# Performance work log

Hardware: AMD Instinct MI355X
Metric: run time of the kernel (lower is better)

The kernel has to match this reference:

```python
import jax, jax.numpy as jnp
import numpy as np

N_NODES = 50000
N_EDGES = 1600000
H_DIM = 128
OUT_DIM = 128
N_RELS = 16


def setup_inputs() -> dict:
    key = jax.random.key(0)
    k1, k2, k3, k4, k5, k6 = jax.random.split(key, 6)
    node_ids = jnp.arange(N_NODES, dtype=jnp.int64) if jax.config.jax_enable_x64 else jnp.arange(N_NODES, dtype=jnp.int32)
    src = jax.random.randint(k1, (N_EDGES,), 0, N_NODES, dtype=jnp.int32)
    dst = jax.random.randint(k2, (N_EDGES,), 0, N_NODES, dtype=jnp.int32)
    rel = jax.random.randint(k3, (N_EDGES,), 0, N_RELS, dtype=jnp.int32)
    norm = jax.random.uniform(k4, (N_EDGES, 1), dtype=jnp.float32)
    emb_table = jax.random.normal(k5, (N_NODES, H_DIM), dtype=jnp.float32)
    W = jax.random.normal(k6, (N_RELS, H_DIM, OUT_DIM), dtype=jnp.float32) * (1.0 / np.sqrt(H_DIM))
    return {"node_ids": node_ids, "src": src, "dst": dst, "rel": rel,
            "norm": norm, "emb_table": emb_table, "W": W}


def reference(node_ids, src, dst, rel, norm, emb_table, W):
    # Input layer: embedding lookup on node ids.  [N, h_dim]
    h = emb_table[node_ids]
    n_nodes = emb_table.shape[0]
    # RelGraphConv (full per-relation weight, no basis, no self-loop,
    # activation=None for the single/last layer, dropout inactive at eval):
    # Transform all node features by every relation weight up front
    # (R small, avoids [E, d, o] per-edge weight gather).  [R, N, out]
    h_rel = jnp.einsum('nd,rdo->rno', h, W)
    # Gather per-edge transformed source features, apply edge norm.  [E, out]
    msg = h_rel[rel, src] * norm
    # Scatter-sum messages to destination nodes.  [N, out]
    out = jax.ops.segment_sum(msg, dst, num_segments=n_nodes)
    return out
```

## Files before the change

kernel.cpp:

```cpp
#include <hip/hip_runtime.h>
#include <hip/hip_bf16.h>

#define NN 50000
#define NE 1600000
#define HD 128
#define NR 16
#define NCB 1563
#define SLOT 2048
#define LASTCAP 1024
#define NMAX 1999
#define PREPH_BLKS 6250
#define PREPW_BLKS 128
#define S2B 512
#define EPB (NE / S2B)

typedef __bf16 bf16x8 __attribute__((ext_vector_type(8)));
typedef unsigned short u16x8 __attribute__((ext_vector_type(8)));
typedef float f32x4 __attribute__((ext_vector_type(4)));

__device__ __forceinline__ unsigned short f2bf(float f) {
    union { float f; unsigned int u; } v; v.f = f;
    unsigned int u = v.u;
    u += 0x7FFFu + ((u >> 16) & 1u);
    return (unsigned short)(u >> 16);
}
__device__ __forceinline__ float bflo(unsigned int u) {
    union { unsigned int u; float f; } v; v.u = u << 16; return v.f;
}
__device__ __forceinline__ float bfhi(unsigned int u) {
    union { unsigned int u; float f; } v; v.u = u & 0xFFFF0000u; return v.f;
}

__global__ __launch_bounds__(256) void prep_all(const int* __restrict__ node_ids,
                                                const float* __restrict__ emb,
                                                unsigned short* __restrict__ h_bf,
                                                const float* __restrict__ W,
                                                unsigned short* __restrict__ Wt,
                                                int* __restrict__ gcur) {
    const int b = blockIdx.x;
    const int t = threadIdx.x;
    if (b < PREPH_BLKS) {
        int gid = b * 256 + t;
        int row = gid >> 5;
        int c = (gid & 31) << 2;
        int nid = node_ids[row];
        if (nid < 0) nid = 0; if (nid >= NN) nid = NN - 1;
        float4 v = *(const float4*)(emb + (size_t)nid * HD + c);
        ushort4 o;
        o.x = f2bf(v.x); o.y = f2bf(v.y); o.z = f2bf(v.z); o.w = f2bf(v.w);
        *(ushort4*)(h_bf + (size_t)row * HD + c) = o;
    } else if (b < PREPH_BLKS + PREPW_BLKS) {
        int gid = (b - PREPH_BLKS) * 256 + t;
        int out8 = gid * 8;
        int r = out8 >> 14;
        int rem = out8 & 16383;
        int o = rem >> 7;
        int k0 = rem & 127;
        const float* wsrc = W + (size_t)r * 16384;
        unsigned short v8[8];
        #pragma unroll
        for (int i = 0; i < 8; ++i)
            v8[i] = f2bf(wsrc[(k0 + i) * 128 + o]);
        *(uint4*)(Wt + (size_t)r * 16384 + (size_t)o * 128 + k0) =
            *(const uint4*)v8;
    } else {
        for (int i = t; i < NCB; i += 256) gcur[i] = 0;
    }
}

__global__ __launch_bounds__(256) void scat2(const int* __restrict__ src,
                                             const int* __restrict__ dst,
                                             const int* __restrict__ rel,
                                             const float* __restrict__ norm,
                                             int* __restrict__ gcur,
                                             uint2* __restrict__ recs) {
    __shared__ int cur[NCB];
    const int t = threadIdx.x, sb = blockIdx.x;
    const int base = sb * EPB;
    for (int i = t; i < NCB; i += 256) cur[i] = 0;
    __syncthreads();
    for (int i = t; i < EPB; i += 256)
        atomicAdd(&cur[((unsigned)dst[base + i]) >> 5], 1);
    __syncthreads();
    for (int i = t; i < NCB; i += 256) {
        int c = cur[i];
        if (c > 0) cur[i] = atomicAdd(&gcur[i], c);
    }
    __syncthreads();
    for (int i = t; i < EPB; i += 256) {
        int e = base + i;
        int d = dst[e];
        int bin = ((unsigned)d) >> 5;
        int p = atomicAdd(&cur[bin], 1);
        int cap = (bin == NCB - 1) ? LASTCAP : SLOT;
        if (p < cap) {
            unsigned x = (unsigned)src[e] | ((unsigned)rel[e] << 16)
                       | ((unsigned)(d & 31) << 20);
            recs[(size_t)bin * SLOT + p] = make_uint2(x, __float_as_uint(norm[e]));
        }
    }
}

__global__ __launch_bounds__(256) void gemm_hrel(const unsigned short* __restrict__ h_bf,
                                                 const unsigned short* __restrict__ Wt,
                                                 unsigned short* __restrict__ h_rel) {
    __shared__ unsigned short sA[128][136];
    __shared__ unsigned short sB[128][136];
    const int t = threadIdx.x;
    const int base = blockIdx.x * 128;
    const int rg = blockIdx.y;

    #pragma unroll
    for (int j = 0; j < 8; ++j) {
        int idx = t + j * 256;
        int row = idx >> 4;
        int c8 = (idx & 15) << 3;
        int g = base + row;
        if (g >= NN) g = 0;
        uint4 v = *(const uint4*)(h_bf + (size_t)g * 128 + c8);
        *(uint4*)&sA[row][c8] = v;
    }

    const int lane = t & 63;
    const int w = t >> 6;
    const int wr = w >> 1, wc = w & 1;
    const int l15 = lane & 15, lhi = lane >> 4;

    for (int rr = 0; rr < 4; ++rr) {
        const int r = rg * 4 + rr;
        if (rr > 0) __syncthreads();
        const unsigned short* wp = Wt + ((size_t)r << 14);
        #pragma unroll
        for (int j = 0; j < 8; ++j) {
            int idx = t + j * 256;
            int row = idx >> 4;
            int c8 = (idx & 15) << 3;
            uint4 v = *(const uint4*)(wp + (size_t)row * 128 + c8);
            *(uint4*)&sB[row][c8] = v;
        }
        __syncthreads();

        f32x4 acc[4][4];
        #pragma unroll
        for (int i = 0; i < 4; ++i)
            #pragma unroll
            for (int j = 0; j < 4; ++j)
                acc[i][j] = (f32x4){0.f, 0.f, 0.f, 0.f};

        #pragma unroll
        for (int kt = 0; kt < 4; ++kt) {
            const int ko = kt * 32 + lhi * 8;
            bf16x8 aF[4], bF[4];
            #pragma unroll
            for (int ms = 0; ms < 4; ++ms) {
                u16x8 raw = *(const u16x8*)&sA[wr * 64 + ms * 16 + l15][ko];
                aF[ms] = __builtin_bit_cast(bf16x8, raw);
            }
            #pragma unroll
            for (int nt = 0; nt < 4; ++nt) {
                u16x8 raw = *(const u16x8*)&sB[wc * 64 + nt * 16 + l15][ko];
                bF[nt] = __builtin_bit_cast(bf16x8, raw);
            }
            #pragma unroll
            for (int ms = 0; ms < 4; ++ms)
                #pragma unroll
                for (int nt = 0; nt < 4; ++nt)
                    acc[ms][nt] = __builtin_amdgcn_mfma_f32_16x16x32_bf16(
                        aF[ms], bF[nt], acc[ms][nt], 0, 0, 0);
        }

        __syncthreads();
        #pragma unroll
        for (int ms = 0; ms < 4; ++ms)
            #pragma unroll
            for (int nt = 0; nt < 4; ++nt)
                #pragma unroll
                for (int reg = 0; reg < 4; ++reg)
                    sB[wr * 64 + ms * 16 + lhi * 4 + reg]
                      [wc * 64 + nt * 16 + l15] = f2bf(acc[ms][nt][reg]);
        __syncthreads();
        size_t rbase = ((size_t)r * NN + base) * 128;
        #pragma unroll
        for (int j = 0; j < 8; ++j) {
            int idx = t + j * 256;
            int row = idx >> 4;
            int c8 = (idx & 15) << 3;
            if (base + row < NN) {
                uint4 v = *(const uint4*)&sB[row][c8];
                *(uint4*)(h_rel + rbase + (size_t)row * 128 + c8) = v;
            }
        }
    }
}

__global__ __launch_bounds__(256, 8) void seg_fused(const int* __restrict__ gcur,
                                                    const uint2* __restrict__ recs,
                                                    const unsigned int* __restrict__ hb,
                                                    float* __restrict__ out) {
    __shared__ uint2 rec[SLOT];
    __shared__ unsigned short idx16[SLOT];
    int* scr = (int*)&rec[NMAX];
    const int t = threadIdx.x;
    const int bin = blockIdx.x;
    const uint2* rg = recs + (size_t)bin * SLOT;
    const int lane = t & 63;
    const int w = t >> 6;

    int n = gcur[bin];
    int cap = (bin == NCB - 1) ? LASTCAP : SLOT;
    if (n > cap) n = cap;
    if (n > NMAX) n = NMAX;

    if (t < 32) scr[t] = 0;
    __syncthreads();
    for (int i = t; i < n; i += 256) {
        uint2 rc = rg[i];
        unsigned row = ((rc.x >> 16) & 15u) * (unsigned)NN + (rc.x & 0xFFFFu);
        rec[i] = make_uint2((rc.x & 0x1F00000u) | row, rc.y);
        atomicAdd(&scr[(rc.x >> 20) & 31u], 1);
    }
    __syncthreads();
    if (t == 0) {
        int acc = 0;
        #pragma unroll
        for (int s = 0; s < 32; ++s) { scr[32 + s] = acc; acc += scr[s]; }
        scr[64] = acc;
    }
    __syncthreads();
    if (t < 32) scr[65 + t] = scr[32 + t];
    __syncthreads();
    for (int i = t; i < n; i += 256) {
        int p = atomicAdd(&scr[65 + (rec[i].x >> 20)], 1);
        idx16[p] = (unsigned short)i;
    }
    __syncthreads();

    #pragma unroll
    for (int k = 0; k < 8; ++k) {
        int j = w * 8 + k;
        int d = bin * 32 + j;
        if (d >= NN) continue;
        int beg = scr[32 + j], end = scr[33 + j];
        float a0 = 0.f, a1 = 0.f;
        int i = beg;
        for (; i + 7 < end; i += 8) {
            int i0 = idx16[i],     i1 = idx16[i + 1];
            int i2 = idx16[i + 2], i3 = idx16[i + 3];
            int i4 = idx16[i + 4], i5 = idx16[i + 5];
            int i6 = idx16[i + 6], i7 = idx16[i + 7];
            uint2 r0 = rec[i0], r1 = rec[i1], r2 = rec[i2], r3 = rec[i3];
            uint2 r4 = rec[i4], r5 = rec[i5], r6 = rec[i6], r7 = rec[i7];
            unsigned u0 = hb[(r0.x & 0xFFFFFu) * 64u + lane];
            unsigned u1 = hb[(r1.x & 0xFFFFFu) * 64u + lane];
            unsigned u2 = hb[(r2.x & 0xFFFFFu) * 64u + lane];
            unsigned u3 = hb[(r3.x & 0xFFFFFu) * 64u + lane];
            unsigned u4 = hb[(r4.x & 0xFFFFFu) * 64u + lane];
            unsigned u5 = hb[(r5.x & 0xFFFFFu) * 64u + lane];
            unsigned u6 = hb[(r6.x & 0xFFFFFu) * 64u + lane];
            unsigned u7 = hb[(r7.x & 0xFFFFFu) * 64u + lane];
            float n0 = __uint_as_float(r0.y), n1 = __uint_as_float(r1.y);
            float n2 = __uint_as_float(r2.y), n3 = __uint_as_float(r3.y);
            float n4 = __uint_as_float(r4.y), n5 = __uint_as_float(r5.y);
            float n6 = __uint_as_float(r6.y), n7 = __uint_as_float(r7.y);
            a0 += bflo(u0) * n0 + bflo(u1) * n1 + bflo(u2) * n2 + bflo(u3) * n3;
            a1 += bfhi(u0) * n0 + bfhi(u1) * n1 + bfhi(u2) * n2 + bfhi(u3) * n3;
            a0 += bflo(u4) * n4 + bflo(u5) * n5 + bflo(u6) * n6 + bflo(u7) * n7;
            a1 += bfhi(u4) * n4 + bfhi(u5) * n5 + bfhi(u6) * n6 + bfhi(u7) * n7;
        }
        for (; i < end; ++i) {
            uint2 rc = rec[idx16[i]];
            unsigned u = hb[(rc.x & 0xFFFFFu) * 64u + lane];
            float nm = __uint_as_float(rc.y);
            a0 += bflo(u) * nm;
            a1 += bfhi(u) * nm;
        }
        *(float2*)(out + (size_t)d * 128 + lane * 2) = make_float2(a0, a1);
    }
}


extern "C" void kernel_launch(void* const* d_in, const int* in_sizes, int n_in,
                              void* d_out, int out_size, void* d_ws, size_t ws_size,
                              hipStream_t stream) {
    const int* node_ids = (const int*)d_in[0];
    const int* src      = (const int*)d_in[1];
    const int* dst      = (const int*)d_in[2];
    const int* rel      = (const int*)d_in[3];
    const float* norm   = (const float*)d_in[4];
    const float* emb    = (const float*)d_in[5];
    const float* W      = (const float*)d_in[6];
    float* out = (float*)d_out;

    char* ws = (char*)d_ws;
    unsigned short* h_rel = (unsigned short*)(ws);
    unsigned short* h_bf  = (unsigned short*)(ws + 204800000);
    unsigned short* Wt    = (unsigned short*)(ws + 217600000);
    int* gcur             = (int*)(ws + 218124288);

    uint2* recs = (uint2*)d_out;

    prep_all<<<PREPH_BLKS + PREPW_BLKS + 1, 256, 0, stream>>>(
        node_ids, emb, h_bf, W, Wt, gcur);
    scat2<<<S2B, 256, 0, stream>>>(src, dst, rel, norm, gcur, recs);
    gemm_hrel<<<dim3(391, 4), 256, 0, stream>>>(h_bf, Wt, h_rel);
    seg_fused<<<NCB, 256, 0, stream>>>(gcur, recs,
                                       (const unsigned int*)h_rel, out);
}
```

Before: 296.9 us.

## Fuse edge binning into prep kernel and split bin counters into slices

Merges the edge scatter/binning kernel into the prep kernel as extra blocks, so one launch is removed and binning can overlap with the embedding and weight conversion. The per-bin global counter is split into 8 slices, each with its own fixed sub-capacity of 256 records, to spread global atomic contention. The segment kernel reads the per-slice counts and gathers the records from each slice. The zeroing of the counters moves to a memset. Fixed per-slice capacity risks dropping edges when a slice overflows, and the fused kernel now allocates shared memory for the prep blocks too.

```diff
diff --git a/kernel.cpp b/kernel.cpp
--- a/kernel.cpp
+++ b/kernel.cpp
@@ -6,8 +6,9 @@
 #define HD 128
 #define NR 16
 #define NCB 1563
+#define NSL 8
+#define SCAP2 256
 #define SLOT 2048
-#define LASTCAP 1024
 #define NMAX 1999
 #define PREPH_BLKS 6250
 #define PREPW_BLKS 128
@@ -31,12 +32,18 @@
     union { unsigned int u; float f; } v; v.u = u & 0xFFFF0000u; return v.f;
 }
 
-__global__ __launch_bounds__(256) void prep_all(const int* __restrict__ node_ids,
-                                                const float* __restrict__ emb,
-                                                unsigned short* __restrict__ h_bf,
-                                                const float* __restrict__ W,
-                                                unsigned short* __restrict__ Wt,
-                                                int* __restrict__ gcur) {
+__global__ __launch_bounds__(256) void prep_scat(const int* __restrict__ node_ids,
+                                                 const float* __restrict__ emb,
+                                                 unsigned short* __restrict__ h_bf,
+                                                 const float* __restrict__ W,
+                                                 unsigned short* __restrict__ Wt,
+                                                 const int* __restrict__ src,
+                                                 const int* __restrict__ dst,
+                                                 const int* __restrict__ rel,
+                                                 const float* __restrict__ norm,
+                                                 int* __restrict__ gcur,
+                                                 uint2* __restrict__ recs) {
+    __shared__ int cur[NCB];
     const int b = blockIdx.x;
     const int t = threadIdx.x;
     if (b < PREPH_BLKS) {
@@ -64,39 +71,31 @@
         *(uint4*)(Wt + (size_t)r * 16384 + (size_t)o * 128 + k0) =
             *(const uint4*)v8;
     } else {
-        for (int i = t; i < NCB; i += 256) gcur[i] = 0;
-    }
-}
-
-__global__ __launch_bounds__(256) void scat2(const int* __restrict__ src,
-                                             const int* __restrict__ dst,
-                                             const int* __restrict__ rel,
-                                             const float* __restrict__ norm,
-                                             int* __restrict__ gcur,
-                                             uint2* __restrict__ recs) {
-    __shared__ int cur[NCB];
-    const int t = threadIdx.x, sb = blockIdx.x;
-    const int base = sb * EPB;
-    for (int i = t; i < NCB; i += 256) cur[i] = 0;
-    __syncthreads();
-    for (int i = t; i < EPB; i += 256)
-        atomicAdd(&cur[((unsigned)dst[base + i]) >> 5], 1);
-    __syncthreads();
-    for (int i = t; i < NCB; i += 256) {
-        int c = cur[i];
-        if (c > 0) cur[i] = atomicAdd(&gcur[i], c);
-    }
-    __syncthreads();
-    for (int i = t; i < EPB; i += 256) {
-        int e = base + i;
-        int d = dst[e];
-        int bin = ((unsigned)d) >> 5;
-        int p = atomicAdd(&cur[bin], 1);
-        int cap = (bin == NCB - 1) ? LASTCAP : SLOT;
-        if (p < cap) {
-            unsigned x = (unsigned)src[e] | ((unsigned)rel[e] << 16)
-                       | ((unsigned)(d & 31) << 20);
-            recs[(size_t)bin * SLOT + p] = make_uint2(x, __float_as_uint(norm[e]));
+        const int sb = b - (PREPH_BLKS + PREPW_BLKS);
+        const int slice = sb & (NSL - 1);
+        const int base = sb * EPB;
+        for (int i = t; i < NCB; i += 256) cur[i] = 0;
+        __syncthreads();
+        for (int i = t; i < EPB; i += 256)
+            atomicAdd(&cur[((unsigned)dst[base + i]) >> 5], 1);
+        __syncthreads();
+        for (int i = t; i < NCB; i += 256) {
+            int c = cur[i];
+            if (c > 0) cur[i] = atomicAdd(&gcur[i * NSL + slice], c);
+        }
+        __syncthreads();
+        for (int i = t; i < EPB; i += 256) {
+            int e = base + i;
+            int d = dst[e];
+            int bin = ((unsigned)d) >> 5;
+            int p = atomicAdd(&cur[bin], 1);
+            int cap2 = (bin == NCB - 1) ? 128 : SCAP2;
+            if (p < cap2) {
+                unsigned x = (unsigned)src[e] | ((unsigned)rel[e] << 16)
+                           | ((unsigned)(d & 31) << 20);
+                recs[(size_t)bin * SLOT + slice * cap2 + p] =
+                    make_uint2(x, __float_as_uint(norm[e]));
+            }
         }
     }
 }
@@ -205,19 +204,35 @@
     const uint2* rg = recs + (size_t)bin * SLOT;
     const int lane = t & 63;
     const int w = t >> 6;
-
-    int n = gcur[bin];
-    int cap = (bin == NCB - 1) ? LASTCAP : SLOT;
-    if (n > cap) n = cap;
-    if (n > NMAX) n = NMAX;
+    const int cap2 = (bin == NCB - 1) ? 128 : SCAP2;
+
+    int c8[NSL], soff[NSL];
+    int run = 0;
+    #pragma unroll
+    for (int s = 0; s < NSL; ++s) {
+        int c = gcur[bin * NSL + s];
+        c8[s] = c > cap2 ? cap2 : c;
+        soff[s] = run;
+        run += c8[s];
+    }
+    const int n = run > NMAX ? NMAX : run;
 
     if (t < 32) scr[t] = 0;
     __syncthreads();
-    for (int i = t; i < n; i += 256) {
-        uint2 rc = rg[i];
-        unsigned row = ((rc.x >> 16) & 15u) * (unsigned)NN + (rc.x & 0xFFFFu);
-        rec[i] = make_uint2((rc.x & 0x1F00000u) | row, rc.y);
-        atomicAdd(&scr[(rc.x >> 20) & 31u], 1);
+    #pragma unroll
+    for (int s = 0; s < NSL; ++s) {
+        if ((s & 3) == w) {
+            for (int idx = lane; idx < c8[s]; idx += 64) {
+                int i = soff[s] + idx;
+                if (i < NMAX) {
+                    uint2 rc = rg[s * cap2 + idx];
+                    unsigned row = ((rc.x >> 16) & 15u) * (unsigned)NN
+                                 + (rc.x & 0xFFFFu);
+                    rec[i] = make_uint2((rc.x & 0x1F00000u) | row, rc.y);
+                    atomicAdd(&scr[(rc.x >> 20) & 31u], 1);
+                }
+            }
+        }
     }
     __syncthreads();
     if (t == 0) {
@@ -299,9 +314,9 @@
 
     uint2* recs = (uint2*)d_out;
 
-    prep_all<<<PREPH_BLKS + PREPW_BLKS + 1, 256, 0, stream>>>(
-        node_ids, emb, h_bf, W, Wt, gcur);
-    scat2<<<S2B, 256, 0, stream>>>(src, dst, rel, norm, gcur, recs);
+    hipMemsetAsync(gcur, 0, NCB * NSL * sizeof(int), stream);
+    prep_scat<<<PREPH_BLKS + PREPW_BLKS + S2B, 256, 0, stream>>>(
+        node_ids, emb, h_bf, W, Wt, src, dst, rel, norm, gcur, recs);
     gemm_hrel<<<dim3(391, 4), 256, 0, stream>>>(h_bf, Wt, h_rel);
     seg_fused<<<NCB, 256, 0, stream>>>(gcur, recs,
                                        (const unsigned int*)h_rel, out);
```

Result: slower. 317.4 us (+6.9%).
